# Kernel tuning notes

Hardware: AMD Instinct MI355X
Metric: run time of the kernel (lower is better)

Reference implementation:

```python
import jax, jax.numpy as jnp
import numpy as np

N, E = 50000, 400000
F_IN, HID, OUT, H = 128, 64, 40, 4
SLOPE = 0.2


def setup_inputs() -> dict:
    key = jax.random.key(0)
    ks = jax.random.split(key, 20)

    def gn(k, shape, scale=0.05):
        return jax.random.normal(k, shape, dtype=jnp.float32) * scale

    inp = {
        "node_inputs": jax.random.normal(ks[0], (N, F_IN), dtype=jnp.float32),
        "src": jax.random.randint(ks[1], (E,), 0, N),
        "dst": jax.random.randint(ks[2], (E,), 0, N),
    }
    # (in_dim, per-head out_dim) per layer; residual linear only when in != heads*out
    dims = [(F_IN, HID), (H * HID, HID), (H * HID, OUT)]
    i = 3
    for l, (fin, d) in enumerate(dims):
        inp[f"w_src{l}"] = gn(ks[i], (fin, H * d)); i += 1
        inp[f"b_src{l}"] = jnp.zeros((H * d,), jnp.float32)
        inp[f"w_dst{l}"] = gn(ks[i], (fin, H * d)); i += 1
        inp[f"b_dst{l}"] = jnp.zeros((H * d,), jnp.float32)
        inp[f"attn{l}"] = gn(ks[i], (H, d)); i += 1
        if fin != H * d:
            inp[f"w_res{l}"] = gn(ks[i], (fin, H * d)); i += 1
            inp[f"b_res{l}"] = jnp.zeros((H * d,), jnp.float32)
    return inp


def _gatv2_layer(x, src, dst, w_s, b_s, w_d, b_d, attn, res):
    # x: [N, F]; res: [N, H*D] residual term (already projected or identity)
    n = x.shape[0]
    h, d = attn.shape
    hs = (x @ w_s + b_s).reshape(n, h, d)   # feat_src
    hd = (x @ w_d + b_d).reshape(n, h, d)   # feat_dst
    e = hs[src] + hd[dst]                    # [E, H, D]
    e = jnp.where(e > 0, e, SLOPE * e)       # LeakyReLU
    logits = jnp.einsum('ehd,hd->eh', e, attn)  # [E, H]
    # edge softmax over incoming edges of each dst node
    m = jax.ops.segment_max(logits, dst, num_segments=n)
    z = jnp.exp(logits - m[dst])
    s = jax.ops.segment_sum(z, dst, num_segments=n)
    a = z / s[dst]                            # [E, H]
    out = jax.ops.segment_sum(hs[src] * a[:, :, None], dst, num_segments=n)  # [N, H, D]
    return out + res.reshape(n, h, d)


def reference(node_inputs, src, dst,
              w_src0, b_src0, w_dst0, b_dst0, attn0, w_res0, b_res0,
              w_src1, b_src1, w_dst1, b_dst1, attn1,
              w_src2, b_src2, w_dst2, b_dst2, attn2, w_res2, b_res2):
    x = node_inputs
    # layer 0: in=128 != heads*hid -> linear residual
    x = _gatv2_layer(x, src, dst, w_src0, b_src0, w_dst0, b_dst0, attn0,
                     x @ w_res0 + b_res0)
    x = x.reshape(x.shape[0], -1)  # flatten heads
    # layer 1: in == heads*hid -> identity residual
    x = _gatv2_layer(x, src, dst, w_src1, b_src1, w_dst1, b_dst1, attn1, x)
    x = x.reshape(x.shape[0], -1)
    # layer 2: in=256 != heads*out -> linear residual
    x = _gatv2_layer(x, src, dst, w_src2, b_src2, w_dst2, b_dst2, attn2,
                     x @ w_res2 + b_res2)
    # mean over heads: [N, H, OUT] -> [N, OUT]
    return x.mean(axis=-2)
```

## Files before the change

kernel.cpp:

```cpp
#include <hip/hip_runtime.h>
#include <hip/hip_bf16.h>
#include <math.h>

#define SLOPE 0.2f

typedef unsigned short bf16_t;
typedef short bh8 __attribute__((ext_vector_type(8)));
typedef unsigned short us8 __attribute__((ext_vector_type(8)));
typedef float f32x4 __attribute__((ext_vector_type(4)));

__device__ __forceinline__ float bf2f(bf16_t x) {
    return __uint_as_float((unsigned)x << 16);
}
__device__ __forceinline__ bf16_t f2bf(float v) {
    unsigned u = __float_as_uint(v);
    return (bf16_t)((u + 0x7FFFu + ((u >> 16) & 1u)) >> 16);
}
__device__ __forceinline__ ushort2 pk_f2bf(float a, float b) {
    __hip_bfloat162 h2 = __float22bfloat162_rn(float2{a, b});
    union { __hip_bfloat162 h; ushort2 u; } u;
    u.h = h2;
    return u.u;
}


__global__ void hist_and_convert(
    const int* __restrict__ dst, int E, int eblocks, int* __restrict__ deg,
    const float* __restrict__ w0, const float* __restrict__ w1, const float* __restrict__ w2,
    const float* __restrict__ w3, const float* __restrict__ w4,
    const float* __restrict__ w5, const float* __restrict__ w6,
    const float* __restrict__ wr2, const float* __restrict__ br2,
    bf16_t* __restrict__ t0, bf16_t* __restrict__ t1, bf16_t* __restrict__ t2,
    bf16_t* __restrict__ t3, bf16_t* __restrict__ t4,
    bf16_t* __restrict__ t5, bf16_t* __restrict__ t6,
    bf16_t* __restrict__ teff, float* __restrict__ b_eff)
{
    int t = threadIdx.x;
    if ((int)blockIdx.x < eblocks) {
        int e = blockIdx.x * 256 + t;
        if (e < E) atomicAdd(&deg[dst[e]], 1);
        return;
    }
    int b = blockIdx.x - eblocks;
    const float* W; bf16_t* T; int K, Nc, lb;
    if (b < 384) {
        int g = b / 128; lb = b - g * 128;
        W = g == 0 ? w0 : (g == 1 ? w1 : w2);
        T = g == 0 ? t0 : (g == 1 ? t1 : t2);
        K = 128; Nc = 256;
    } else if (b < 896) {
        int g = (b - 384) / 256; lb = (b - 384) - g * 256;
        W = g == 0 ? w3 : w4; T = g == 0 ? t3 : t4;
        K = 256; Nc = 256;
    } else if (b < 1280) {
        int g = (b - 896) / 192; lb = (b - 896) - g * 192;
        W = g == 0 ? w5 : w6; T = g == 0 ? t5 : t6;
        K = 256; Nc = 160;
    } else {
        lb = b - 1280;
        int idx = lb * 256 + t;
        int n = idx >> 8, k = idx & 255;
        float v = 0.f;
        if (n < 40)
            v = 0.25f * (wr2[(size_t)k * 160 + n] + wr2[(size_t)k * 160 + 40 + n] +
                         wr2[(size_t)k * 160 + 80 + n] + wr2[(size_t)k * 160 + 120 + n]);
        teff[idx] = f2bf(v);
        if (lb == 0 && t < 40)
            b_eff[t] = 0.25f * (br2[t] + br2[40 + t] + br2[80 + t] + br2[120 + t]);
        return;
    }
    int idx = lb * 256 + t;
    int n = idx / K, k = idx - n * K;
    float v = (n < Nc) ? W[(size_t)k * Nc + n] : 0.f;
    T[idx] = f2bf(v);
}


__global__ void deg_chunk_sum(const int* __restrict__ deg, int n, int* __restrict__ chunk_sums) {
    __shared__ int sm[256];
    int base = blockIdx.x * 1024;
    int s = 0;
    for (int i = threadIdx.x; i < 1024; i += 256) {
        int idx = base + i;
        if (idx < n) s += deg[idx];
    }
    sm[threadIdx.x] = s;
    __syncthreads();
    for (int off = 128; off > 0; off >>= 1) {
        if (threadIdx.x < off) sm[threadIdx.x] += sm[threadIdx.x + off];
        __syncthreads();
    }
    if (threadIdx.x == 0) chunk_sums[blockIdx.x] = sm[0];
}

__global__ void scan_write(const int* __restrict__ deg, int n,
                           const int* __restrict__ chunk_sums,
                           int* __restrict__ row_start, int Etot) {
    __shared__ int sm[256];
    __shared__ int s_pref;
    int base = blockIdx.x * 1024;
    int t = threadIdx.x;

    if (t < 64) {
        int v = (t < (int)blockIdx.x) ? chunk_sums[t] : 0;
#pragma unroll
        for (int off = 32; off > 0; off >>= 1)
            v += __shfl_down(v, off, 64);
        if (t == 0) s_pref = v;
    }

    int vv[4];
    int tsum = 0;
#pragma unroll
    for (int j = 0; j < 4; j++) {
        int idx = base + t * 4 + j;
        vv[j] = (idx < n) ? deg[idx] : 0;
        tsum += vv[j];
    }
    sm[t] = tsum;
    __syncthreads();
    for (int off = 1; off < 256; off <<= 1) {
        int x = (t >= off) ? sm[t - off] : 0;
        __syncthreads();
        sm[t] += x;
        __syncthreads();
    }
    int excl = sm[t] - tsum + s_pref;
#pragma unroll
    for (int j = 0; j < 4; j++) {
        int idx = base + t * 4 + j;
        if (idx < n) row_start[idx] = excl;
        excl += vv[j];
    }
    if (blockIdx.x == 0 && t == 0) row_start[n] = Etot;
}


template <typename TA, int NOUT, int KTOT, int NPAD, bool SPLIT40, bool HAS_EFF, bool DO_SCATTER>
__global__ __launch_bounds__(256) void gemm_lds(
    const TA* __restrict__ A,
    const bf16_t* __restrict__ Wt0, const bf16_t* __restrict__ Wt1, const bf16_t* __restrict__ Wt2,
    const float* __restrict__ bias0, const float* __restrict__ bias1, const float* __restrict__ bias2,
    bf16_t* __restrict__ C0, bf16_t* __restrict__ C1, bf16_t* __restrict__ C2,
    const bf16_t* __restrict__ Wte, const float* __restrict__ biase, float* __restrict__ Ce,
    int M, int Nc,
    const int* __restrict__ e_dst, const int* __restrict__ e_src, int E,
    const int* __restrict__ row_start, int* __restrict__ fill,
    int* __restrict__ src_sorted, int mtiles)
{
    constexpr int LSTR = KTOT + 8;
    constexpr int ESTR = 38;
    constexpr int KC = KTOT / 32;
    __shared__ bf16_t As[64 * LSTR];
    __shared__ bf16_t Ep[4 * 64 * ESTR];

    int tid = threadIdx.x;

    if (DO_SCATTER && (int)blockIdx.x >= mtiles) {
        int e = (blockIdx.x - mtiles) * 256 + tid;
        if (e < E) {
            int d_ = e_dst[e];
            int pos = row_start[d_] + atomicAdd(&fill[d_], 1);
            src_sorted[pos] = e_src[e];
        }
        return;
    }

    int lane = tid & 63, w = tid >> 6;
    int lm = lane & 15, lq = lane >> 4;
    int m0 = blockIdx.x * 64;

    const bf16_t* Wts[3] = {Wt0, Wt1, Wt2};
    const float* biases[3] = {bias0, bias1, bias2};
    bf16_t* Cs[3] = {C0, C1, C2};

    if (sizeof(TA) == 4) {
#pragma unroll
        for (int it = 0; it < 4; it++) {
            int idx = tid + it * 256;
            int r = idx >> 4, c = idx & 15;
            int gm = m0 + r; if (gm >= M) gm = M - 1;
            const float* ap = (const float*)A + (size_t)gm * KTOT + c * 8;
            float4 lo = *(const float4*)ap;
            float4 hi = *(const float4*)(ap + 4);
            ushort2 p0 = pk_f2bf(lo.x, lo.y), p1 = pk_f2bf(lo.z, lo.w);
            ushort2 p2 = pk_f2bf(hi.x, hi.y), p3 = pk_f2bf(hi.z, hi.w);
            bh8 v = { (short)p0.x, (short)p0.y, (short)p1.x, (short)p1.y,
                      (short)p2.x, (short)p2.y, (short)p3.x, (short)p3.y };
            *(bh8*)(As + r * LSTR + c * 8) = v;
        }
    } else {
#pragma unroll
        for (int it = 0; it < 8; it++) {
            int idx = tid + it * 256;
            int r = idx >> 5, c = idx & 31;
            int gm = m0 + r; if (gm >= M) gm = M - 1;
            bh8 v = *(const bh8*)((const bf16_t*)A + (size_t)gm * KTOT + c * 8);
            *(bh8*)(As + r * LSTR + c * 8) = v;
        }
    }
    __syncthreads();

    bf16_t* ep = Ep + w * (64 * ESTR);
    constexpr int NCHUNK = (NPAD + 127) / 128;

#pragma unroll
    for (int chunk = 0; chunk < NCHUNK; chunk++) {
        int n0 = chunk * 128 + w * 32;
        if (n0 >= NPAD) continue;

        int boff[NOUT][2];
#pragma unroll
        for (int o = 0; o < NOUT; o++)
#pragma unroll
            for (int nt = 0; nt < 2; nt++)
                boff[o][nt] = (n0 + nt * 16 + lm) * KTOT + lq * 8;

        f32x4 acc[NOUT][4][2];
#pragma unroll
        for (int o = 0; o < NOUT; o++)
#pragma unroll
            for (int i = 0; i < 4; i++)
#pragma unroll
                for (int j = 0; j < 2; j++)
                    acc[o][i][j] = (f32x4){0.f, 0.f, 0.f, 0.f};

        bh8 bf_cur[NOUT][2], bf_nxt[NOUT][2];
#pragma unroll
        for (int o = 0; o < NOUT; o++)
#pragma unroll
            for (int nt = 0; nt < 2; nt++)
                bf_cur[o][nt] = *(const bh8*)(Wts[o] + boff[o][nt]);

#pragma unroll
        for (int kc = 0; kc < KC; kc++) {
            if (kc + 1 < KC) {
#pragma unroll
                for (int o = 0; o < NOUT; o++)
#pragma unroll
                    for (int nt = 0; nt < 2; nt++)
                        bf_nxt[o][nt] = *(const bh8*)(Wts[o] + boff[o][nt] + (kc + 1) * 32);
            }
            bh8 af[4];
#pragma unroll
            for (int mt = 0; mt < 4; mt++)
                af[mt] = *(const bh8*)(As + (mt * 16 + lm) * LSTR + kc * 32 + lq * 8);
#pragma unroll
            for (int o = 0; o < NOUT; o++)
#pragma unroll
                for (int mt = 0; mt < 4; mt++)
#pragma unroll
                    for (int nt = 0; nt < 2; nt++)
                        acc[o][mt][nt] = __builtin_amdgcn_mfma_f32_16x16x32_bf16(af[mt], bf_cur[o][nt], acc[o][mt][nt], 0, 0, 0);
            if (kc + 1 < KC) {
#pragma unroll
                for (int o = 0; o < NOUT; o++)
#pragma unroll
                    for (int nt = 0; nt < 2; nt++)
                        bf_cur[o][nt] = bf_nxt[o][nt];
            }
        }

#pragma unroll
        for (int o = 0; o < NOUT; o++) {
#pragma unroll
            for (int nt = 0; nt < 2; nt++) {
                int gn = n0 + nt * 16 + lm;
                float bv = (gn < Nc) ? biases[o][gn] : 0.f;
#pragma unroll
                for (int mt = 0; mt < 4; mt++)
#pragma unroll
                    for (int r = 0; r < 4; r++)
                        ep[(mt * 16 + lq * 4 + r) * ESTR + nt * 16 + lm] = f2bf(acc[o][mt][nt][r] + bv);
            }
#pragma unroll
            for (int it = 0; it < 4; it++) {
                int row = it * 16 + (lane >> 2);
                int cc = (lane & 3) * 8;
                bh8 v = *(const bh8*)(ep + row * ESTR + cc);
                int gm = m0 + row;
                int cg = n0 + cc;
                if (gm < M && cg < Nc) {
                    size_t cb = SPLIT40 ? (size_t)(cg + 24 * (cg / 40)) : (size_t)cg;
                    size_t rs = SPLIT40 ? 256 : (size_t)Nc;
                    *(bh8*)(Cs[o] + (size_t)gm * rs + cb) = v;
                }
            }
        }
    }

    if (HAS_EFF && w < 2) {
        int beoff[2];
#pragma unroll
        for (int nt = 0; nt < 2; nt++)
            beoff[nt] = (w * 32 + nt * 16 + lm) * KTOT + lq * 8;
        f32x4 acc_e[4][2];
#pragma unroll
        for (int i = 0; i < 4; i++)
#pragma unroll
            for (int j = 0; j < 2; j++)
                acc_e[i][j] = (f32x4){0.f, 0.f, 0.f, 0.f};
#pragma unroll
        for (int kc = 0; kc < KC; kc++) {
            bh8 af[4];
#pragma unroll
            for (int mt = 0; mt < 4; mt++)
                af[mt] = *(const bh8*)(As + (mt * 16 + lm) * LSTR + kc * 32 + lq * 8);
            bh8 be[2];
#pragma unroll
            for (int nt = 0; nt < 2; nt++)
                be[nt] = *(const bh8*)(Wte + beoff[nt] + kc * 32);
#pragma unroll
            for (int mt = 0; mt < 4; mt++)
#pragma unroll
                for (int nt = 0; nt < 2; nt++)
                    acc_e[mt][nt] = __builtin_amdgcn_mfma_f32_16x16x32_bf16(af[mt], be[nt], acc_e[mt][nt], 0, 0, 0);
        }
#pragma unroll
        for (int nt = 0; nt < 2; nt++) {
            int gn = w * 32 + nt * 16 + lm;
            if (gn >= 40) continue;
            float bv = biase[gn];
#pragma unroll
            for (int mt = 0; mt < 4; mt++)
#pragma unroll
                for (int r = 0; r < 4; r++) {
                    int gm = m0 + mt * 16 + lq * 4 + r;
                    if (gm < M) Ce[(size_t)gm * 40 + gn] = acc_e[mt][nt][r] + bv;
                }
        }
    }
}


__device__ __forceinline__ void us8_to_f(const us8 v, float* h) {
#pragma unroll
    for (int j = 0; j < 8; j++) h[j] = bf2f(v[j]);
}

__device__ __forceinline__ float edge_logit16(const float h[16], const float hdf[16], const float at[16]) {
    float p = 0.f;
#pragma unroll
    for (int j = 0; j < 16; j++) {
        float q = h[j] + hdf[j];
        p += fmaxf(q, SLOPE * q) * at[j];
    }
    p += __shfl_xor(p, 1, 64);
    p += __shfl_xor(p, 2, 64);
    return p;
}

template <int DVALID, bool FINAL, bool RES_INPLACE>
__global__ __launch_bounds__(256) void gat_agg_quarter(
    const bf16_t* __restrict__ hs, const bf16_t* __restrict__ hd,
    const float* __restrict__ attn,
    const int* __restrict__ row_start, const int* __restrict__ src_sorted,
    bf16_t* __restrict__ P, float* __restrict__ out_final, int N)
{
    int w = threadIdx.x >> 6, lane = threadIdx.x & 63;
    int q = lane >> 4, ql = lane & 15;
    int n = blockIdx.x * 16 + w * 4 + q;
    if (n >= N) return;
    int f0 = ql * 16;
    int h = ql >> 2;
    int dp = (ql & 3) * 16;

    float at[16], hdf[16];
#pragma unroll
    for (int j = 0; j < 16; j++)
        at[j] = (dp + j < DVALID) ? attn[h * DVALID + dp + j] : 0.f;
    {
        us8 a = *(const us8*)(hd + (unsigned)(n * 256 + f0));
        us8 b = *(const us8*)(hd + (unsigned)(n * 256 + f0 + 8));
        us8_to_f(a, hdf); us8_to_f(b, hdf + 8);
    }

    float pc;
    {
        float p = 0.f;
#pragma unroll
        for (int j = 0; j < 16; j++) {
            float qq = hdf[j];
            p += fmaxf(qq, SLOPE * qq) * at[j];
        }
        p += __shfl_xor(p, 1, 64);
        p += __shfl_xor(p, 2, 64);
        pc = p;
    }

    int s = row_start[n], e = row_start[n + 1];

    float cl0 = 0.f, cl1 = 0.f;
    float ca0[16] = {}, ca1[16] = {};

    int i = s;
    for (; i + 2 <= e; i += 2) {
        int sn0 = src_sorted[i], sn1 = src_sorted[i + 1];
        us8 r0a = *(const us8*)(hs + (unsigned)(sn0 * 256 + f0));
        us8 r0b = *(const us8*)(hs + (unsigned)(sn0 * 256 + f0 + 8));
        us8 r1a = *(const us8*)(hs + (unsigned)(sn1 * 256 + f0));
        us8 r1b = *(const us8*)(hs + (unsigned)(sn1 * 256 + f0 + 8));
        float h0[16], h1[16];
        us8_to_f(r0a, h0); us8_to_f(r0b, h0 + 8);
        us8_to_f(r1a, h1); us8_to_f(r1b, h1 + 8);
        float w0 = __expf(edge_logit16(h0, hdf, at) - pc);
        float w1 = __expf(edge_logit16(h1, hdf, at) - pc);
        cl0 += w0; cl1 += w1;
#pragma unroll
        for (int j = 0; j < 16; j++) {
            ca0[j] += w0 * h0[j];
            ca1[j] += w1 * h1[j];
        }
    }
    if (i < e) {
        int sn0 = src_sorted[i];
        us8 r0a = *(const us8*)(hs + (unsigned)(sn0 * 256 + f0));
        us8 r0b = *(const us8*)(hs + (unsigned)(sn0 * 256 + f0 + 8));
        float h0[16];
        us8_to_f(r0a, h0); us8_to_f(r0b, h0 + 8);
        float w0 = __expf(edge_logit16(h0, hdf, at) - pc);
        cl0 += w0;
#pragma unroll
        for (int j = 0; j < 16; j++) ca0[j] += w0 * h0[j];
    }

    float v[16] = {};
    if (e > s) {
        float inv = 1.f / (cl0 + cl1);
#pragma unroll
        for (int j = 0; j < 16; j++)
            v[j] = (ca0[j] + ca1[j]) * inv;
    }

    if (FINAL) {
#pragma unroll
        for (int j = 0; j < 16; j++) {
            v[j] += __shfl_xor(v[j], 4, 64);
            v[j] += __shfl_xor(v[j], 8, 64);
        }
        if (h == 0) {
#pragma unroll
            for (int jj = 0; jj < 16; jj += 4) {
                if (dp + jj < DVALID) {
                    float* op = out_final + (unsigned)(n * DVALID + dp + jj);
                    float4 cur = *(float4*)op;
                    cur.x += 0.25f * v[jj];
                    cur.y += 0.25f * v[jj + 1];
                    cur.z += 0.25f * v[jj + 2];
                    cur.w += 0.25f * v[jj + 3];
                    *(float4*)op = cur;
                }
            }
        }
    } else {
        unsigned oi = (unsigned)(n * 256 + f0);
        if (RES_INPLACE) {
            us8 pa = *(const us8*)(P + oi);
            us8 pb = *(const us8*)(P + oi + 8);
#pragma unroll
            for (int j = 0; j < 8; j++) {
                v[j] += bf2f(pa[j]);
                v[8 + j] += bf2f(pb[j]);
            }
        }
        us8 oa, ob;
#pragma unroll
        for (int j = 0; j < 8; j++) {
            oa[j] = f2bf(v[j]);
            ob[j] = f2bf(v[8 + j]);
        }
        *(us8*)(P + oi) = oa;
        *(us8*)(P + oi + 8) = ob;
    }
}


extern "C" void kernel_launch(void* const* d_in, const int* in_sizes, int n_in,
                              void* d_out, int out_size, void* d_ws, size_t ws_size,
                              hipStream_t stream) {
    const float* x0    = (const float*)d_in[0];
    const int*   src   = (const int*)d_in[1];
    const int*   dst   = (const int*)d_in[2];
    const float* w_src0 = (const float*)d_in[3];  const float* b_src0 = (const float*)d_in[4];
    const float* w_dst0 = (const float*)d_in[5];  const float* b_dst0 = (const float*)d_in[6];
    const float* attn0  = (const float*)d_in[7];
    const float* w_res0 = (const float*)d_in[8];  const float* b_res0 = (const float*)d_in[9];
    const float* w_src1 = (const float*)d_in[10]; const float* b_src1 = (const float*)d_in[11];
    const float* w_dst1 = (const float*)d_in[12]; const float* b_dst1 = (const float*)d_in[13];
    const float* attn1  = (const float*)d_in[14];
    const float* w_src2 = (const float*)d_in[15]; const float* b_src2 = (const float*)d_in[16];
    const float* w_dst2 = (const float*)d_in[17]; const float* b_dst2 = (const float*)d_in[18];
    const float* attn2  = (const float*)d_in[19];
    const float* w_res2 = (const float*)d_in[20]; const float* b_res2 = (const float*)d_in[21];

    const int N = in_sizes[0] / 128;
    const int E = in_sizes[1];
    float* out = (float*)d_out;
    (void)n_in; (void)out_size; (void)ws_size;

    char* ws = (char*)d_ws;
    size_t off = 0;
    auto alloc = [&](size_t bytes) {
        void* q = ws + off;
        off = (off + bytes + 255) & ~(size_t)255;
        return q;
    };
    int* deg        = (int*)alloc((size_t)2 * N * 4);
    int* fill       = deg + N;
    int* row_start  = (int*)alloc((size_t)(N + 1) * 4);
    int* chunk_sums = (int*)alloc(256 * 4);
    int* src_sorted = (int*)alloc((size_t)E * 4);
    bf16_t* t_src0 = (bf16_t*)alloc(256 * 128 * 2);
    bf16_t* t_dst0 = (bf16_t*)alloc(256 * 128 * 2);
    bf16_t* t_res0 = (bf16_t*)alloc(256 * 128 * 2);
    bf16_t* t_src1 = (bf16_t*)alloc(256 * 256 * 2);
    bf16_t* t_dst1 = (bf16_t*)alloc(256 * 256 * 2);
    bf16_t* t_src2 = (bf16_t*)alloc(192 * 256 * 2);
    bf16_t* t_dst2 = (bf16_t*)alloc(192 * 256 * 2);
    bf16_t* t_eff  = (bf16_t*)alloc(64 * 256 * 2);
    float*  b_eff  = (float*)alloc(64 * 4);
    const size_t elems = (size_t)N * 256;
    bf16_t* P  = (bf16_t*)alloc(elems * 2);
    bf16_t* HS = (bf16_t*)alloc(elems * 2);
    bf16_t* HD = (bf16_t*)alloc(elems * 2);

    hipMemsetAsync(deg, 0, (size_t)2 * N * 4, stream);
    int eblocks = (E + 255) / 256;
    int nchunks = (N + 1023) / 1024;
    hipLaunchKernelGGL(hist_and_convert, dim3(eblocks + 1344), dim3(256), 0, stream,
                       dst, E, eblocks, deg,
                       w_src0, w_dst0, w_res0, w_src1, w_dst1, w_src2, w_dst2, w_res2, b_res2,
                       t_src0, t_dst0, t_res0, t_src1, t_dst1, t_src2, t_dst2, t_eff, b_eff);
    hipLaunchKernelGGL(deg_chunk_sum, dim3(nchunks), dim3(256), 0, stream, deg, N, chunk_sums);
    hipLaunchKernelGGL(scan_write, dim3(nchunks), dim3(256), 0, stream, deg, N, chunk_sums, row_start, E);

    dim3 blk(256);
    int mtiles = (N + 63) / 64;
    int ab = (N + 15) / 16;

    hipLaunchKernelGGL((gemm_lds<float, 3, 128, 256, false, false, true>),
                       dim3(mtiles + eblocks), blk, 0, stream,
                       x0, t_src0, t_dst0, t_res0, b_src0, b_dst0, b_res0,
                       HS, HD, P,
                       (const bf16_t*)nullptr, (const float*)nullptr, (float*)nullptr,
                       N, 256,
                       dst, src, E, row_start, fill, src_sorted, mtiles);
    hipLaunchKernelGGL((gat_agg_quarter<64, false, true>), dim3(ab), blk, 0, stream,
                       HS, HD, attn0, row_start, src_sorted, P, (float*)nullptr, N);

    hipLaunchKernelGGL((gemm_lds<bf16_t, 2, 256, 256, false, false, false>), dim3(mtiles), blk, 0, stream,
                       P, t_src1, t_dst1, (const bf16_t*)nullptr, b_src1, b_dst1, (const float*)nullptr,
                       HS, HD, (bf16_t*)nullptr,
                       (const bf16_t*)nullptr, (const float*)nullptr, (float*)nullptr,
                       N, 256,
                       (const int*)nullptr, (const int*)nullptr, 0,
                       (const int*)nullptr, (int*)nullptr, (int*)nullptr, 0);
    hipLaunchKernelGGL((gat_agg_quarter<64, false, true>), dim3(ab), blk, 0, stream,
                       HS, HD, attn1, row_start, src_sorted, P, (float*)nullptr, N);

    hipLaunchKernelGGL((gemm_lds<bf16_t, 2, 256, 192, true, true, false>), dim3(mtiles), blk, 0, stream,
                       P, t_src2, t_dst2, (const bf16_t*)nullptr, b_src2, b_dst2, (const float*)nullptr,
                       HS, HD, (bf16_t*)nullptr,
                       t_eff, b_eff, out,
                       N, 160,
                       (const int*)nullptr, (const int*)nullptr, 0,
                       (const int*)nullptr, (int*)nullptr, (int*)nullptr, 0);
    hipLaunchKernelGGL((gat_agg_quarter<40, true, false>), dim3(ab), blk, 0, stream,
                       HS, HD, attn2, row_start, src_sorted, (bf16_t*)nullptr, out, N);
}
```

Before: 413.2 us.

## Assign one wave per node and split edges across quarter-waves

The aggregation kernel now maps each node to a full wave instead of a quarter-wave. The four quarters process interleaved edges of the same node and combine their partial softmax denominators and weighted sums with cross-lane shuffles. This is meant to shorten the serial per-node edge loop and reduce imbalance from varying degrees. In exchange it launches four times as many waves, duplicates the per-node hd/attn setup, and adds shuffle reductions.

```diff
diff --git a/kernel.cpp b/kernel.cpp
--- a/kernel.cpp
+++ b/kernel.cpp
@@ -351,7 +351,7 @@
 }
 
 template <int DVALID, bool FINAL, bool RES_INPLACE>
-__global__ __launch_bounds__(256) void gat_agg_quarter(
+__global__ __launch_bounds__(256) void gat_agg_wave(
     const bf16_t* __restrict__ hs, const bf16_t* __restrict__ hd,
     const float* __restrict__ attn,
     const int* __restrict__ row_start, const int* __restrict__ src_sorted,
@@ -359,7 +359,7 @@
 {
     int w = threadIdx.x >> 6, lane = threadIdx.x & 63;
     int q = lane >> 4, ql = lane & 15;
-    int n = blockIdx.x * 16 + w * 4 + q;
+    int n = blockIdx.x * 4 + w;
     if (n >= N) return;
     int f0 = ql * 16;
     int h = ql >> 2;
@@ -393,9 +393,9 @@
     float cl0 = 0.f, cl1 = 0.f;
     float ca0[16] = {}, ca1[16] = {};
 
-    int i = s;
-    for (; i + 2 <= e; i += 2) {
-        int sn0 = src_sorted[i], sn1 = src_sorted[i + 1];
+    int i = s + q;
+    for (; i + 4 < e; i += 8) {
+        int sn0 = src_sorted[i], sn1 = src_sorted[i + 4];
         us8 r0a = *(const us8*)(hs + (unsigned)(sn0 * 256 + f0));
         us8 r0b = *(const us8*)(hs + (unsigned)(sn0 * 256 + f0 + 8));
         us8 r1a = *(const us8*)(hs + (unsigned)(sn1 * 256 + f0));
@@ -424,12 +424,18 @@
         for (int j = 0; j < 16; j++) ca0[j] += w0 * h0[j];
     }
 
-    float v[16] = {};
-    if (e > s) {
-        float inv = 1.f / (cl0 + cl1);
-#pragma unroll
-        for (int j = 0; j < 16; j++)
-            v[j] = (ca0[j] + ca1[j]) * inv;
+    float cl = cl0 + cl1;
+    cl += __shfl_xor(cl, 16, 64);
+    cl += __shfl_xor(cl, 32, 64);
+
+    float v[16];
+    float inv = (e > s) ? 1.f / cl : 0.f;
+#pragma unroll
+    for (int j = 0; j < 16; j++) {
+        float c = ca0[j] + ca1[j];
+        c += __shfl_xor(c, 16, 64);
+        c += __shfl_xor(c, 32, 64);
+        v[j] = c * inv;
     }
 
     if (FINAL) {
@@ -438,7 +444,7 @@
             v[j] += __shfl_xor(v[j], 4, 64);
             v[j] += __shfl_xor(v[j], 8, 64);
         }
-        if (h == 0) {
+        if (q == 0 && h == 0) {
 #pragma unroll
             for (int jj = 0; jj < 16; jj += 4) {
                 if (dp + jj < DVALID) {
@@ -452,7 +458,7 @@
                 }
             }
         }
-    } else {
+    } else if (q == 0) {
         unsigned oi = (unsigned)(n * 256 + f0);
         if (RES_INPLACE) {
             us8 pa = *(const us8*)(P + oi);
@@ -536,7 +542,7 @@
 
     dim3 blk(256);
     int mtiles = (N + 63) / 64;
-    int ab = (N + 15) / 16;
+    int ab = (N + 3) / 4;
 
     hipLaunchKernelGGL((gemm_lds<float, 3, 128, 256, false, false, true>),
                        dim3(mtiles + eblocks), blk, 0, stream,
@@ -545,7 +551,7 @@
                        (const bf16_t*)nullptr, (const float*)nullptr, (float*)nullptr,
                        N, 256,
                        dst, src, E, row_start, fill, src_sorted, mtiles);
-    hipLaunchKernelGGL((gat_agg_quarter<64, false, true>), dim3(ab), blk, 0, stream,
+    hipLaunchKernelGGL((gat_agg_wave<64, false, true>), dim3(ab), blk, 0, stream,
                        HS, HD, attn0, row_start, src_sorted, P, (float*)nullptr, N);
 
     hipLaunchKernelGGL((gemm_lds<bf16_t, 2, 256, 256, false, false, false>), dim3(mtiles), blk, 0, stream,
@@ -555,7 +561,7 @@
                        N, 256,
                        (const int*)nullptr, (const int*)nullptr, 0,
                        (const int*)nullptr, (int*)nullptr, (int*)nullptr, 0);
-    hipLaunchKernelGGL((gat_agg_quarter<64, false, true>), dim3(ab), blk, 0, stream,
+    hipLaunchKernelGGL((gat_agg_wave<64, false, true>), dim3(ab), blk, 0, stream,
                        HS, HD, attn1, row_start, src_sorted, P, (float*)nullptr, N);
 
     hipLaunchKernelGGL((gemm_lds<bf16_t, 2, 256, 192, true, true, false>), dim3(mtiles), blk, 0, stream,
@@ -565,6 +571,6 @@
                        N, 160,
                        (const int*)nullptr, (const int*)nullptr, 0,
                        (const int*)nullptr, (int*)nullptr, (int*)nullptr, 0);
-    hipLaunchKernelGGL((gat_agg_quarter<40, true, false>), dim3(ab), blk, 0, stream,
+    hipLaunchKernelGGL((gat_agg_wave<40, true, false>), dim3(ab), blk, 0, stream,
                        HS, HD, attn2, row_start, src_sorted, (bf16_t*)nullptr, out, N);
 }
```

New measurement: 479.5 us. +16.1%, slower.

## Sort destination nodes by in-degree to balance aggregation wavefronts

Applied to the files above, without the earlier changes.

Builds a degree histogram and a counting-sort permutation of nodes by in-degree (capped at 127) during the CSR scan. Each aggregation kernel then processes nodes in permuted order, so the 16-lane groups sharing a wavefront get similar edge counts. This is meant to cut divergence and idle lanes caused by uneven degrees. In exchange it adds atomics, a serial 128-entry prefix in every scan block, an extra indirection per node, and less locality in hd/P accesses.

```diff
diff --git a/kernel.cpp b/kernel.cpp
--- a/kernel.cpp
+++ b/kernel.cpp
@@ -76,30 +76,47 @@
 }
 
 
-__global__ void deg_chunk_sum(const int* __restrict__ deg, int n, int* __restrict__ chunk_sums) {
+__global__ void deg_chunk_sum(const int* __restrict__ deg, int n,
+                              int* __restrict__ chunk_sums, int* __restrict__ bcnt) {
     __shared__ int sm[256];
+    __shared__ int hl[128];
+    int t = threadIdx.x;
+    if (t < 128) hl[t] = 0;
+    __syncthreads();
     int base = blockIdx.x * 1024;
     int s = 0;
-    for (int i = threadIdx.x; i < 1024; i += 256) {
+    for (int i = t; i < 1024; i += 256) {
         int idx = base + i;
-        if (idx < n) s += deg[idx];
-    }
-    sm[threadIdx.x] = s;
+        if (idx < n) {
+            int d = deg[idx];
+            s += d;
+            atomicAdd(&hl[d < 127 ? d : 127], 1);
+        }
+    }
+    sm[t] = s;
     __syncthreads();
     for (int off = 128; off > 0; off >>= 1) {
-        if (threadIdx.x < off) sm[threadIdx.x] += sm[threadIdx.x + off];
+        if (t < off) sm[t] += sm[t + off];
         __syncthreads();
     }
-    if (threadIdx.x == 0) chunk_sums[blockIdx.x] = sm[0];
+    if (t == 0) chunk_sums[blockIdx.x] = sm[0];
+    if (t < 128 && hl[t]) atomicAdd(&bcnt[t], hl[t]);
 }
 
 __global__ void scan_write(const int* __restrict__ deg, int n,
                            const int* __restrict__ chunk_sums,
-                           int* __restrict__ row_start, int Etot) {
+                           int* __restrict__ row_start, int Etot,
+                           const int* __restrict__ bcnt, int* __restrict__ bfill,
+                           int* __restrict__ perm) {
     __shared__ int sm[256];
     __shared__ int s_pref;
+    __shared__ int sbase[128];
+    __shared__ int lcnt[128];
+    __shared__ int gbase[128];
     int base = blockIdx.x * 1024;
     int t = threadIdx.x;
+
+    if (t < 128) lcnt[t] = 0;
 
     if (t < 64) {
         int v = (t < (int)blockIdx.x) ? chunk_sums[t] : 0;
@@ -107,6 +124,10 @@
         for (int off = 32; off > 0; off >>= 1)
             v += __shfl_down(v, off, 64);
         if (t == 0) s_pref = v;
+    }
+    if (t == 128) {
+        int run = 0;
+        for (int i = 0; i < 128; i++) { sbase[i] = run; run += bcnt[i]; }
     }
 
     int vv[4];
@@ -133,6 +154,25 @@
         excl += vv[j];
     }
     if (blockIdx.x == 0 && t == 0) row_start[n] = Etot;
+
+    int rnk[4], bb[4];
+#pragma unroll
+    for (int j = 0; j < 4; j++) {
+        int idx = base + t * 4 + j;
+        if (idx < n) {
+            bb[j] = vv[j] < 127 ? vv[j] : 127;
+            rnk[j] = atomicAdd(&lcnt[bb[j]], 1);
+        } else bb[j] = -1;
+    }
+    __syncthreads();
+    if (t < 128 && lcnt[t]) gbase[t] = atomicAdd(&bfill[t], lcnt[t]);
+    __syncthreads();
+#pragma unroll
+    for (int j = 0; j < 4; j++) {
+        int idx = base + t * 4 + j;
+        if (bb[j] >= 0)
+            perm[sbase[bb[j]] + gbase[bb[j]] + rnk[j]] = idx;
+    }
 }
 
 
@@ -355,12 +395,14 @@
     const bf16_t* __restrict__ hs, const bf16_t* __restrict__ hd,
     const float* __restrict__ attn,
     const int* __restrict__ row_start, const int* __restrict__ src_sorted,
+    const int* __restrict__ perm,
     bf16_t* __restrict__ P, float* __restrict__ out_final, int N)
 {
     int w = threadIdx.x >> 6, lane = threadIdx.x & 63;
     int q = lane >> 4, ql = lane & 15;
-    int n = blockIdx.x * 16 + w * 4 + q;
-    if (n >= N) return;
+    int gq = blockIdx.x * 16 + w * 4 + q;
+    if (gq >= N) return;
+    int n = perm[gq];
     int f0 = ql * 16;
     int h = ql >> 2;
     int dp = (ql & 3) * 16;
@@ -507,6 +549,9 @@
     };
     int* deg        = (int*)alloc((size_t)2 * N * 4);
     int* fill       = deg + N;
+    int* bcnt       = (int*)alloc(256 * 4);
+    int* bfill      = bcnt + 128;
+    int* perm       = (int*)alloc((size_t)N * 4);
     int* row_start  = (int*)alloc((size_t)(N + 1) * 4);
     int* chunk_sums = (int*)alloc(256 * 4);
     int* src_sorted = (int*)alloc((size_t)E * 4);
@@ -525,14 +570,16 @@
     bf16_t* HD = (bf16_t*)alloc(elems * 2);
 
     hipMemsetAsync(deg, 0, (size_t)2 * N * 4, stream);
+    hipMemsetAsync(bcnt, 0, 256 * 4, stream);
     int eblocks = (E + 255) / 256;
     int nchunks = (N + 1023) / 1024;
     hipLaunchKernelGGL(hist_and_convert, dim3(eblocks + 1344), dim3(256), 0, stream,
                        dst, E, eblocks, deg,
                        w_src0, w_dst0, w_res0, w_src1, w_dst1, w_src2, w_dst2, w_res2, b_res2,
                        t_src0, t_dst0, t_res0, t_src1, t_dst1, t_src2, t_dst2, t_eff, b_eff);
-    hipLaunchKernelGGL(deg_chunk_sum, dim3(nchunks), dim3(256), 0, stream, deg, N, chunk_sums);
-    hipLaunchKernelGGL(scan_write, dim3(nchunks), dim3(256), 0, stream, deg, N, chunk_sums, row_start, E);
+    hipLaunchKernelGGL(deg_chunk_sum, dim3(nchunks), dim3(256), 0, stream, deg, N, chunk_sums, bcnt);
+    hipLaunchKernelGGL(scan_write, dim3(nchunks), dim3(256), 0, stream, deg, N, chunk_sums,
+                       row_start, E, bcnt, bfill, perm);
 
     dim3 blk(256);
     int mtiles = (N + 63) / 64;
@@ -546,7 +593,7 @@
                        N, 256,
                        dst, src, E, row_start, fill, src_sorted, mtiles);
     hipLaunchKernelGGL((gat_agg_quarter<64, false, true>), dim3(ab), blk, 0, stream,
-                       HS, HD, attn0, row_start, src_sorted, P, (float*)nullptr, N);
+                       HS, HD, attn0, row_start, src_sorted, perm, P, (float*)nullptr, N);
 
     hipLaunchKernelGGL((gemm_lds<bf16_t, 2, 256, 256, false, false, false>), dim3(mtiles), blk, 0, stream,
                        P, t_src1, t_dst1, (const bf16_t*)nullptr, b_src1, b_dst1, (const float*)nullptr,
@@ -556,7 +603,7 @@
                        (const int*)nullptr, (const int*)nullptr, 0,
                        (const int*)nullptr, (int*)nullptr, (int*)nullptr, 0);
     hipLaunchKernelGGL((gat_agg_quarter<64, false, true>), dim3(ab), blk, 0, stream,
-                       HS, HD, attn1, row_start, src_sorted, P, (float*)nullptr, N);
+                       HS, HD, attn1, row_start, src_sorted, perm, P, (float*)nullptr, N);
 
     hipLaunchKernelGGL((gemm_lds<bf16_t, 2, 256, 192, true, true, false>), dim3(mtiles), blk, 0, stream,
                        P, t_src2, t_dst2, (const bf16_t*)nullptr, b_src2, b_dst2, (const float*)nullptr,
@@ -566,5 +613,5 @@
                        (const int*)nullptr, (const int*)nullptr, 0,
                        (const int*)nullptr, (int*)nullptr, (int*)nullptr, 0);
     hipLaunchKernelGGL((gat_agg_quarter<40, true, false>), dim3(ab), blk, 0, stream,
-                       HS, HD, attn2, row_start, src_sorted, (bf16_t*)nullptr, out, N);
-}
+                       HS, HD, attn2, row_start, src_sorted, perm, (bf16_t*)nullptr, out, N);
+}
```

After: 415.0 us. No clear change (+0.5%).
